# Kernel optimization log

Measured on AMD Instinct MI355X. Metric: run time of the kernel, lower is better.

Reference implementation:

```python
import jax, jax.numpy as jnp
import numpy as np

N = 2048  # device_num
K = 32    # neighbors per device


def setup_inputs() -> dict:
    key = jax.random.key(0)
    k1, k2, k3 = jax.random.split(key, 3)
    dynamic_re = jax.random.uniform(k1, (N, N), dtype=jnp.float32)
    static_re = jax.random.uniform(k2, (N,), dtype=jnp.float32)
    # neighbor ids in [0, N) excluding self (draw in [0, N-1) then shift past row index)
    r = jax.random.randint(k3, (N, K), 0, N - 1)
    rows = jnp.arange(N)[:, None]
    neighbor_matrix = (r + (r >= rows)).astype(jnp.int32)
    return {"dynamic_re": dynamic_re, "static_re": static_re, "neighbor_matrix": neighbor_matrix}


def _trust_forward(dynamic_re, static_re, neighbor_matrix):
    # Semantics of RobustTrustComputing.__call__ on a fresh instance (temp_storage empty):
    #  - diagonal: 1.0
    #  - neighbor (j in nbr(i)): history has len 1 -> CI branch is False -> combined
    #    tau = 0.7*dyn[i,j] + 0.3*stat[j]; prev==combined -> hysteresis takes the
    #    'x <= prev' path: sigmoid(combined + 0.5) with sigmoid(z)=(1-e^-z)/(1+e^-z)=tanh(z/2)
    #  - non-neighbor with common neighbors c: 0.8 * mean_c rep[i,c]*rep[c,j] read from the
    #    PARTIALLY-FILLED matrix in row-major write order (rep[i,c] nonzero only if c<j,
    #    rep[c,j] nonzero only if c<i); divisor is the FULL common-neighbor count.
    #  - non-neighbor, no common neighbors: 0.5*stat[j]
    #  - final clamp to [0,1]
    n = dynamic_re.shape[0]
    idx = jnp.arange(n)
    # membership matrix: M[i, c] True iff c appears in neighbor list of i
    M = jnp.zeros((n, n), dtype=bool).at[idx[:, None], neighbor_matrix].set(True)
    nbrval = jnp.tanh(0.5 * (0.7 * dynamic_re + 0.3 * static_re[None, :] + 0.5))
    Mf = M.astype(dynamic_re.dtype)
    count = Mf @ Mf.T                                  # |common neighbors(i, j)|
    Bmask = Mf.T * (idx[:, None] < idx[None, :])       # [c, j]: c in nbr(j) AND c < j
    fallback = 0.5 * static_re                         # [j]

    def step(rep, xs):
        i, M_i, nbr_i, cnt_i = xs
        # rep[i, c] (c in nbr(i)) equals nbrval[i, c] once column c has been written (c < j,
        # handled by Bmask); rep[c, j] is the final row c only for c < i (rows >= i are zero).
        A = jnp.where(M_i & (idx < i), nbr_i, 0.0)     # [c]
        num = jnp.einsum('c,cj,cj->j', A, rep, Bmask)  # [j]
        indirect = 0.8 * num / jnp.maximum(cnt_i, 1.0)
        row = jnp.where(M_i, nbr_i, jnp.where(cnt_i > 0, indirect, fallback))
        row = jnp.where(idx == i, 1.0, row)            # diagonal overrides everything
        return rep.at[i].set(row), None

    rep0 = jnp.zeros((n, n), dynamic_re.dtype)
    rep, _ = jax.lax.scan(step, rep0, (idx, M, nbrval, count))
    return jnp.clip(rep, 0.0, 1.0)


def reference(dynamic_re, static_re, neighbor_matrix):
    return _trust_forward(dynamic_re, static_re, neighbor_matrix)
```

## Files before the change

### kernel.cpp

```cpp
#include <hip/hip_runtime.h>
#include <math.h>
#include <limits.h>

#define WAVE 64
#define KMAX 32
#define IMAX 96

__device__ __forceinline__ float nvval(float d, float s) {
    float z = 0.7f * d + 0.3f * s + 0.5f;
    float e = __expf(z);
    return 1.0f - 2.0f / (e + 1.0f);
}
__device__ __forceinline__ float clamp01(float x) {
    return fminf(fmaxf(x, 0.0f), 1.0f);
}

__global__ void build_lists(const int* __restrict__ nbr, int N, int K, int W,
                            int* __restrict__ nbrs_sorted, int* __restrict__ deg,
                            unsigned* __restrict__ Mbits,
                            int* __restrict__ invcnt, int* __restrict__ invlist,
                            int* __restrict__ invpos) {
    int tid = blockIdx.x * blockDim.x + threadIdx.x;
    int i = tid / WAVE;
    int lane = tid % WAVE;
    if (i >= N) return;
    bool have = (lane < K);
    int val = have ? nbr[(size_t)i * K + lane] : INT_MAX;
    bool dup = false;
    unsigned mybits = 0;
    #pragma unroll
    for (int t = 0; t < KMAX; ++t) {
        int vt = __shfl(val, t);
        if (have && t < lane && vt == val) dup = true;
        if ((vt >> 5) == lane) mybits |= 1u << (vt & 31);
    }
    if (lane < W) Mbits[(size_t)i * W + lane] = mybits;
    int dupi = (dup || !have) ? 1 : 0;
    int pos = 0;
    #pragma unroll
    for (int t = 0; t < KMAX; ++t) {
        int vt = __shfl(val, t);
        int dt = __shfl(dupi, t);
        if (!dt && vt < val) pos++;
    }
    int myp = (have && !dup) ? pos : -1;
    unsigned long long m = __ballot(have && !dup);
    int degv = __popcll(m);
    int slot = INT_MAX;
    #pragma unroll
    for (int t = 0; t < KMAX; ++t) {
        int pt = __shfl(myp, t);
        int vt = __shfl(val, t);
        if (pt == lane) slot = vt;
    }
    if (lane < K) nbrs_sorted[(size_t)i * K + lane] = slot;
    if (lane == 0) deg[i] = degv;
    if (have && !dup) {
        int p = atomicAdd(&invcnt[val], 1);
        if (p < IMAX) invlist[(size_t)val * IMAX + p] = i;
        invpos[(size_t)i * K + myp] = p;
    }
}

__global__ void __launch_bounds__(256) phase1(
        const float* __restrict__ dyn, const float* __restrict__ stat,
        const int* __restrict__ nbrs_sorted, const int* __restrict__ deg,
        const unsigned* __restrict__ Mbits,
        const int* __restrict__ invpos, int N, int K, int W,
        float* __restrict__ Vcomp) {
    __shared__ float s_nv[4 * KMAX * KMAX];
    int tid = blockIdx.x * blockDim.x + threadIdx.x;
    int j = tid / WAVE;
    int lane = threadIdx.x & (WAVE - 1);
    int waveid = threadIdx.x >> 6;
    if (j >= N) return;
    int degj = deg[j];
    int c = (lane < K) ? nbrs_sorted[(size_t)j * K + lane] : INT_MAX;
    bool validk = (lane < degj);
    float sk = validk ? stat[c] : 0.0f;
    float statj = stat[j];
    float* s_row = &s_nv[waveid * KMAX * KMAX];

    unsigned dirbit = 0;
    if (validk) {
        unsigned w = Mbits[(size_t)c * W + (j >> 5)];
        dirbit = (w >> (j & 31)) & 1u;
    }
    unsigned dirmask = (unsigned)__ballot(dirbit != 0);
    float dv = 0.0f;
    if (dirbit) dv = nvval(dyn[(size_t)c * N + j], statj);

    unsigned hmAll = 0;
    #pragma unroll
    for (int m = 0; m < KMAX; ++m) {
        int cm = __shfl(c, m);
        if (cm < N) {
            unsigned w = validk ? Mbits[(size_t)cm * W + (c >> 5)] : 0u;
            unsigned b = (w >> (c & 31)) & 1u;
            hmAll |= b << m;
            if (b && lane < m && c < j)
                s_row[m * KMAX + lane] = nvval(dyn[(size_t)cm * N + c], sk);
        }
    }
    unsigned lm = (lane < 31) ? (0xFFFFFFFEu << lane) : 0u;
    unsigned hmTerm = (validk && c < j) ? (hmAll & lm) : 0u;

    int mycnt = 0;
    unsigned H = 0;
    #pragma unroll
    for (int m = 0; m < KMAX; ++m) {
        unsigned long long ball = __ballot((hmAll >> m) & 1u);
        unsigned long long ballT = __ballot((hmTerm >> m) & 1u);
        if (lane == m) mycnt = __popcll(ball);
        H |= (ballT ? 1u : 0u) << m;
    }
    H = __builtin_amdgcn_readfirstlane(H);
    dirmask = __builtin_amdgcn_readfirstlane(dirmask);

    float v = 0.0f;
    #pragma unroll
    for (int m = 0; m < KMAX; ++m) {
        float num = 0.0f;
        if (H & (1u << m)) {
            float t = 0.0f;
            if ((hmTerm >> m) & 1u) t = s_row[m * KMAX + lane] * v;
            num = t;
            num += __shfl_xor(num, 16);
            num += __shfl_xor(num, 8);
            num += __shfl_xor(num, 4);
            num += __shfl_xor(num, 2);
            num += __shfl_xor(num, 1);
        }
        float val;
        if ((dirmask >> m) & 1u) val = dv;
        else if (mycnt > 0) val = 0.8f * num / (float)mycnt;
        else val = 0.5f * statj;
        val = clamp01(val);
        if (lane == m) v = val;
    }
    if (validk) {
        int p = invpos[(size_t)j * K + lane];
        if (p < IMAX) Vcomp[(size_t)c * IMAX + p] = v;
    }
}

__global__ void __launch_bounds__(256) phase2(
        const float* __restrict__ dyn, const float* __restrict__ stat,
        const int* __restrict__ nbrs_sorted,
        const int* __restrict__ invcnt, const int* __restrict__ invlist,
        const float* __restrict__ Vcomp,
        int N, int K, float* __restrict__ out) {
    extern __shared__ char smem[];
    int* s_cnt = (int*)smem;
    float* s_num = (float*)(s_cnt + N);
    int* s_nbr = (int*)(s_num + N);
    float* s_nv = (float*)(s_nbr + KMAX);
    int* s_icnt = (int*)(s_nv + KMAX);
    __shared__ int s_me;

    int i = blockIdx.x;
    int tid = threadIdx.x;

    for (int t = tid; t < N; t += blockDim.x) { s_cnt[t] = 0; s_num[t] = 0.0f; }
    if (tid < K) {
        int c = nbrs_sorted[(size_t)i * K + tid];
        s_nbr[tid] = c;
        if (c < N) {
            s_nv[tid] = nvval(dyn[(size_t)i * N + c], stat[c]);
            int m = invcnt[c];
            s_icnt[tid] = (m < IMAX) ? m : IMAX;
        } else {
            s_nv[tid] = 0.0f;
            s_icnt[tid] = 0;
        }
    }
    if (tid == 0) {
        int m = invcnt[i];
        s_me = (m < IMAX) ? m : IMAX;
    }
    __syncthreads();

    {
        int k = tid >> 3;
        int sub = tid & 7;
        if (k < K) {
            int c = s_nbr[k];
            int m = s_icnt[k];
            float nv = s_nv[k];
            if (c < N) {
                const int4* il4 = (const int4*)&invlist[(size_t)c * IMAX];
                const float4* vc4 = (const float4*)&Vcomp[(size_t)c * IMAX];
                for (int base = sub * 4; base < m; base += 32) {
                    int4 js = il4[base >> 2];
                    float4 vs = vc4[base >> 2];
                    int jj[4] = {js.x, js.y, js.z, js.w};
                    float vv[4] = {vs.x, vs.y, vs.z, vs.w};
                    #pragma unroll
                    for (int t = 0; t < 4; ++t) {
                        int e = base + t;
                        if (e < m) {
                            int j = jj[t];
                            atomicAdd(&s_cnt[j], 1);
                            if (c < i && c < j)
                                atomicAdd(&s_num[j], nv * vv[t]);
                        }
                    }
                }
            }
        }
    }
    __syncthreads();

    if (tid < K) {
        int c = s_nbr[tid];
        if (c < N) { s_cnt[c] = -1; s_num[c] = s_nv[tid]; }
    }
    __syncthreads();

    int me = s_me;
    for (int e = tid; e < me; e += blockDim.x) {
        int j = invlist[(size_t)i * IMAX + e];
        s_cnt[j] = -1;
        s_num[j] = Vcomp[(size_t)i * IMAX + e];
    }
    __syncthreads();

    for (int j = tid; j < N; j += blockDim.x) {
        int cnt = s_cnt[j];
        float val;
        if (j == i) val = 1.0f;
        else if (cnt < 0) val = s_num[j];
        else if (cnt > 0) val = 0.8f * s_num[j] / (float)cnt;
        else val = 0.5f * stat[j];
        out[(size_t)i * N + j] = clamp01(val);
    }
}

extern "C" void kernel_launch(void* const* d_in, const int* in_sizes, int n_in,
                              void* d_out, int out_size, void* d_ws, size_t ws_size,
                              hipStream_t stream) {
    const float* dyn = (const float*)d_in[0];
    const float* stat = (const float*)d_in[1];
    const int* nbr = (const int*)d_in[2];
    int N = in_sizes[1];
    int K = in_sizes[2] / N;
    int W = (N + 31) / 32;
    float* out = (float*)d_out;

    char* ws = (char*)d_ws;
    size_t offIC = 0;
    size_t offM = offIC + (size_t)N * sizeof(int);
    size_t offIP = offM + (size_t)N * W * sizeof(unsigned);
    size_t offIL = offIP + (size_t)N * K * sizeof(int);
    size_t offVC = offIL + (size_t)N * IMAX * sizeof(int);
    size_t offNbr = offVC + (size_t)N * IMAX * sizeof(float);
    size_t offDeg = offNbr + (size_t)N * K * sizeof(int);
    int* invcnt = (int*)(ws + offIC);
    unsigned* Mbits = (unsigned*)(ws + offM);
    int* invpos = (int*)(ws + offIP);
    int* invlist = (int*)(ws + offIL);
    float* Vcomp = (float*)(ws + offVC);
    int* nbrs_sorted = (int*)(ws + offNbr);
    int* deg = (int*)(ws + offDeg);

    hipMemsetAsync(ws + offIC, 0, (size_t)N * sizeof(int), stream);

    int threads = 256;
    int blocksWave = (N * WAVE + threads - 1) / threads;
    build_lists<<<blocksWave, threads, 0, stream>>>(nbr, N, K, W, nbrs_sorted, deg,
                                                    Mbits, invcnt, invlist, invpos);
    phase1<<<blocksWave, threads, 0, stream>>>(dyn, stat, nbrs_sorted, deg,
                                               Mbits, invpos, N, K, W, Vcomp);
    size_t smem = (size_t)N * 8 + (size_t)KMAX * 12 + 16;
    phase2<<<N, threads, smem, stream>>>(dyn, stat, nbrs_sorted,
                                         invcnt, invlist, Vcomp, N, K, out);
}
```

Baseline: 115.2 us.

## Fuse list building into phase1 and precompute neighbor values for phase2

Moves the neighbor dedup, sort and inverse-list construction out of the first kernel and into phase1, leaving a minimal bitmask kernel. Phase1 now keeps the atomic slot positions in registers, which removes the invpos and deg arrays. Phase1 also precomputes each row's direct neighbor values (Dval), so phase2 no longer does scattered reads of dyn. This cuts global round trips and intermediate traffic. Masking j with N-1 assumes N is a power of two, and the invlist entries are written while the same kernel also reads them only later in phase2, so ordering across kernels stays safe.

```diff
diff --git a/kernel.cpp b/kernel.cpp
--- a/kernel.cpp
+++ b/kernel.cpp
@@ -15,71 +15,78 @@
     return fminf(fmaxf(x, 0.0f), 1.0f);
 }
 
-__global__ void build_lists(const int* __restrict__ nbr, int N, int K, int W,
-                            int* __restrict__ nbrs_sorted, int* __restrict__ deg,
-                            unsigned* __restrict__ Mbits,
-                            int* __restrict__ invcnt, int* __restrict__ invlist,
-                            int* __restrict__ invpos) {
+__global__ void mbits_kernel(const int* __restrict__ nbr, int N, int K, int W,
+                             unsigned* __restrict__ Mbits) {
     int tid = blockIdx.x * blockDim.x + threadIdx.x;
     int i = tid / WAVE;
-    int lane = tid % WAVE;
+    int lane = tid & (WAVE - 1);
     if (i >= N) return;
-    bool have = (lane < K);
-    int val = have ? nbr[(size_t)i * K + lane] : INT_MAX;
-    bool dup = false;
+    int val = (lane < K) ? nbr[(size_t)i * K + lane] : INT_MAX;
     unsigned mybits = 0;
     #pragma unroll
     for (int t = 0; t < KMAX; ++t) {
         int vt = __shfl(val, t);
-        if (have && t < lane && vt == val) dup = true;
         if ((vt >> 5) == lane) mybits |= 1u << (vt & 31);
     }
     if (lane < W) Mbits[(size_t)i * W + lane] = mybits;
-    int dupi = (dup || !have) ? 1 : 0;
-    int pos = 0;
-    #pragma unroll
-    for (int t = 0; t < KMAX; ++t) {
-        int vt = __shfl(val, t);
-        int dt = __shfl(dupi, t);
-        if (!dt && vt < val) pos++;
-    }
-    int myp = (have && !dup) ? pos : -1;
-    unsigned long long m = __ballot(have && !dup);
-    int degv = __popcll(m);
-    int slot = INT_MAX;
-    #pragma unroll
-    for (int t = 0; t < KMAX; ++t) {
-        int pt = __shfl(myp, t);
-        int vt = __shfl(val, t);
-        if (pt == lane) slot = vt;
-    }
-    if (lane < K) nbrs_sorted[(size_t)i * K + lane] = slot;
-    if (lane == 0) deg[i] = degv;
-    if (have && !dup) {
-        int p = atomicAdd(&invcnt[val], 1);
-        if (p < IMAX) invlist[(size_t)val * IMAX + p] = i;
-        invpos[(size_t)i * K + myp] = p;
-    }
-}
-
-__global__ void __launch_bounds__(256) phase1(
+}
+
+__global__ void __launch_bounds__(256) build_phase1(
         const float* __restrict__ dyn, const float* __restrict__ stat,
-        const int* __restrict__ nbrs_sorted, const int* __restrict__ deg,
-        const unsigned* __restrict__ Mbits,
-        const int* __restrict__ invpos, int N, int K, int W,
-        float* __restrict__ Vcomp) {
+        const int* __restrict__ nbr, const unsigned* __restrict__ Mbits,
+        int N, int K, int W,
+        int* __restrict__ nbrs_sorted, int* __restrict__ invcnt,
+        int* __restrict__ invlist, float* __restrict__ Vcomp,
+        float* __restrict__ Dval) {
     __shared__ float s_nv[4 * KMAX * KMAX];
     int tid = blockIdx.x * blockDim.x + threadIdx.x;
     int j = tid / WAVE;
     int lane = threadIdx.x & (WAVE - 1);
     int waveid = threadIdx.x >> 6;
     if (j >= N) return;
-    int degj = deg[j];
-    int c = (lane < K) ? nbrs_sorted[(size_t)j * K + lane] : INT_MAX;
+    float* s_row = &s_nv[waveid * KMAX * KMAX];
+
+    bool have = (lane < K);
+    int val = have ? nbr[(size_t)j * K + lane] : INT_MAX;
+    bool dup = false;
+    #pragma unroll
+    for (int t = 0; t < KMAX; ++t) {
+        int vt = __shfl(val, t);
+        if (have && t < lane && vt == val) dup = true;
+    }
+    int dupi = (dup || !have) ? 1 : 0;
+    int pos = 0;
+    #pragma unroll
+    for (int t = 0; t < KMAX; ++t) {
+        int vt = __shfl(val, t);
+        int dt = __shfl(dupi, t);
+        if (!dt && vt < val) pos++;
+    }
+    int myp = (have && !dup) ? pos : -1;
+    int degj = __popcll(__ballot(have && !dup));
+
+    int p = -1;
+    if (have && !dup) {
+        p = atomicAdd(&invcnt[val], 1);
+        if (p >= 0 && p < IMAX) invlist[(size_t)val * IMAX + p] = j;
+    }
+
+    int c = INT_MAX;
+    int psort = -1;
+    #pragma unroll
+    for (int t = 0; t < KMAX; ++t) {
+        int pt = __shfl(myp, t);
+        int vt = __shfl(val, t);
+        int pp = __shfl(p, t);
+        if (pt == lane) { c = vt; psort = pp; }
+    }
+    if (lane < K) nbrs_sorted[(size_t)j * K + lane] = c;
     bool validk = (lane < degj);
     float sk = validk ? stat[c] : 0.0f;
     float statj = stat[j];
-    float* s_row = &s_nv[waveid * KMAX * KMAX];
+
+    if (lane < K)
+        Dval[(size_t)j * K + lane] = validk ? nvval(dyn[(size_t)j * N + c], sk) : 0.0f;
 
     unsigned dirbit = 0;
     if (validk) {
@@ -131,24 +138,22 @@
             num += __shfl_xor(num, 2);
             num += __shfl_xor(num, 1);
         }
-        float val;
-        if ((dirmask >> m) & 1u) val = dv;
-        else if (mycnt > 0) val = 0.8f * num / (float)mycnt;
-        else val = 0.5f * statj;
-        val = clamp01(val);
-        if (lane == m) v = val;
-    }
-    if (validk) {
-        int p = invpos[(size_t)j * K + lane];
-        if (p < IMAX) Vcomp[(size_t)c * IMAX + p] = v;
-    }
+        float val2;
+        if ((dirmask >> m) & 1u) val2 = dv;
+        else if (mycnt > 0) val2 = 0.8f * num / (float)mycnt;
+        else val2 = 0.5f * statj;
+        val2 = clamp01(val2);
+        if (lane == m) v = val2;
+    }
+    if (validk && psort >= 0 && psort < IMAX)
+        Vcomp[(size_t)c * IMAX + psort] = v;
 }
 
 __global__ void __launch_bounds__(256) phase2(
-        const float* __restrict__ dyn, const float* __restrict__ stat,
+        const float* __restrict__ stat,
         const int* __restrict__ nbrs_sorted,
         const int* __restrict__ invcnt, const int* __restrict__ invlist,
-        const float* __restrict__ Vcomp,
+        const float* __restrict__ Vcomp, const float* __restrict__ Dval,
         int N, int K, float* __restrict__ out) {
     extern __shared__ char smem[];
     int* s_cnt = (int*)smem;
@@ -165,18 +170,13 @@
     if (tid < K) {
         int c = nbrs_sorted[(size_t)i * K + tid];
         s_nbr[tid] = c;
-        if (c < N) {
-            s_nv[tid] = nvval(dyn[(size_t)i * N + c], stat[c]);
-            int m = invcnt[c];
-            s_icnt[tid] = (m < IMAX) ? m : IMAX;
-        } else {
-            s_nv[tid] = 0.0f;
-            s_icnt[tid] = 0;
-        }
+        s_nv[tid] = Dval[(size_t)i * K + tid];
+        int m = (c < N) ? invcnt[c] : 0;
+        s_icnt[tid] = (m < 0) ? 0 : ((m < IMAX) ? m : IMAX);
     }
     if (tid == 0) {
         int m = invcnt[i];
-        s_me = (m < IMAX) ? m : IMAX;
+        s_me = (m < 0) ? 0 : ((m < IMAX) ? m : IMAX);
     }
     __syncthreads();
 
@@ -199,7 +199,7 @@
                     for (int t = 0; t < 4; ++t) {
                         int e = base + t;
                         if (e < m) {
-                            int j = jj[t];
+                            int j = jj[t] & (N - 1);
                             atomicAdd(&s_cnt[j], 1);
                             if (c < i && c < j)
                                 atomicAdd(&s_num[j], nv * vv[t]);
@@ -219,7 +219,7 @@
 
     int me = s_me;
     for (int e = tid; e < me; e += blockDim.x) {
-        int j = invlist[(size_t)i * IMAX + e];
+        int j = invlist[(size_t)i * IMAX + e] & (N - 1);
         s_cnt[j] = -1;
         s_num[j] = Vcomp[(size_t)i * IMAX + e];
     }
@@ -250,28 +250,26 @@
     char* ws = (char*)d_ws;
     size_t offIC = 0;
     size_t offM = offIC + (size_t)N * sizeof(int);
-    size_t offIP = offM + (size_t)N * W * sizeof(unsigned);
-    size_t offIL = offIP + (size_t)N * K * sizeof(int);
+    size_t offIL = offM + (size_t)N * W * sizeof(unsigned);
     size_t offVC = offIL + (size_t)N * IMAX * sizeof(int);
     size_t offNbr = offVC + (size_t)N * IMAX * sizeof(float);
-    size_t offDeg = offNbr + (size_t)N * K * sizeof(int);
+    size_t offDv = offNbr + (size_t)N * K * sizeof(int);
     int* invcnt = (int*)(ws + offIC);
     unsigned* Mbits = (unsigned*)(ws + offM);
-    int* invpos = (int*)(ws + offIP);
     int* invlist = (int*)(ws + offIL);
     float* Vcomp = (float*)(ws + offVC);
     int* nbrs_sorted = (int*)(ws + offNbr);
-    int* deg = (int*)(ws + offDeg);
+    float* Dval = (float*)(ws + offDv);
 
     hipMemsetAsync(ws + offIC, 0, (size_t)N * sizeof(int), stream);
 
     int threads = 256;
     int blocksWave = (N * WAVE + threads - 1) / threads;
-    build_lists<<<blocksWave, threads, 0, stream>>>(nbr, N, K, W, nbrs_sorted, deg,
-                                                    Mbits, invcnt, invlist, invpos);
-    phase1<<<blocksWave, threads, 0, stream>>>(dyn, stat, nbrs_sorted, deg,
-                                               Mbits, invpos, N, K, W, Vcomp);
+    mbits_kernel<<<blocksWave, threads, 0, stream>>>(nbr, N, K, W, Mbits);
+    build_phase1<<<blocksWave, threads, 0, stream>>>(dyn, stat, nbr, Mbits, N, K, W,
+                                                     nbrs_sorted, invcnt, invlist,
+                                                     Vcomp, Dval);
     size_t smem = (size_t)N * 8 + (size_t)KMAX * 12 + 16;
-    phase2<<<N, threads, smem, stream>>>(dyn, stat, nbrs_sorted,
-                                         invcnt, invlist, Vcomp, N, K, out);
-}
+    phase2<<<N, threads, smem, stream>>>(stat, nbrs_sorted, invcnt, invlist,
+                                         Vcomp, Dval, N, K, out);
+}
```

Result: no change. 115.1 us (-0.1%).
